# Performance work log

Hardware: AMD Instinct MI355X
Metric: run time of the kernel (lower is better)

The kernel has to match this reference:

```python
import jax, jax.numpy as jnp
import numpy as np

B, L, S = 1, 2048, 2048
D_MODEL, H = 1024, 16
DK = D_MODEL // H  # d_keys = d_values = 64


def sparsemax(z):
    # sparsemax along last axis: proj of z onto the simplex
    K = z.shape[-1]
    z_sorted = jnp.flip(jnp.sort(z, axis=-1), axis=-1)
    cs = jnp.cumsum(z_sorted, axis=-1)
    r = jnp.arange(1, K + 1, dtype=z.dtype)
    support = 1.0 + r * z_sorted > cs
    k = jnp.sum(support, axis=-1, keepdims=True)
    tau = (jnp.take_along_axis(cs, k.astype(jnp.int32) - 1, axis=-1) - 1.0) / k.astype(z.dtype)
    return jnp.maximum(z - tau, 0.0)


def setup_inputs() -> dict:
    key = jax.random.key(0)
    ks = jax.random.split(key, 12)
    sc = 1.0 / np.sqrt(D_MODEL)
    return {
        "queries": jax.random.normal(ks[0], (B, L, D_MODEL), jnp.float32),
        "keys": jax.random.normal(ks[1], (B, S, D_MODEL), jnp.float32),
        "values": jax.random.normal(ks[2], (B, S, D_MODEL), jnp.float32),
        "Wq": jax.random.normal(ks[3], (D_MODEL, H * DK), jnp.float32) * sc,
        "bq": jnp.zeros((H * DK,), jnp.float32),
        "Wk": jax.random.normal(ks[4], (D_MODEL, H * DK), jnp.float32) * sc,
        "bk": jnp.zeros((H * DK,), jnp.float32),
        "Wv": jax.random.normal(ks[5], (H * DK, H * DK), jnp.float32) * sc,
        "bv": jnp.zeros((H * DK,), jnp.float32),
        "Wo": jax.random.normal(ks[6], (H * DK, D_MODEL), jnp.float32) * sc,
        "bo": jnp.zeros((D_MODEL,), jnp.float32),
    }


def reference(queries, keys, values, Wq, bq, Wk, bk, Wv, bv, Wo, bo):
    # projections (note: input `values` is unused, matching the torch source)
    q = (queries @ Wq + bq).reshape(B, L, H, DK)
    k_flat = keys @ Wk + bk                      # [B,S,H*DK]
    k = k_flat.reshape(B, S, H, DK)
    v = (k_flat @ Wv + bv).reshape(B, S, H, DK)  # value_projection(key_projection(keys))
    scale = 1.0 / np.sqrt(DK)
    scores = jnp.einsum('blhe,bshe->bhls', q, k) * scale  # [B,H,L,S]
    A = sparsemax(scores)
    out = jnp.einsum('bhls,bshd->blhd', A, v)             # [B,L,H,DK]
    # mix=True: transpose(2,1) -> [B,H,L,D] then view(B,L,-1)
    out = jnp.swapaxes(out, 1, 2).reshape(B, L, H * DK)
    return out @ Wo + bo
```

## Files before the change

### kernel.cpp

```cpp
#include <hip/hip_runtime.h>
#include <hip/hip_bf16.h>


typedef __attribute__((ext_vector_type(8))) short short8;
typedef __attribute__((ext_vector_type(4))) float floatx4;

#define SRC_BF16 0
#define SRC_F32  1
#define SRC_RT   2
#define NSEG 12
#define OVF 64
#define OVBASE 192
#define CAPP 257

typedef __attribute__((address_space(1))) const void GAS;
typedef __attribute__((address_space(3))) void LAS;
#define GLOAD16(g, l) __builtin_amdgcn_global_load_lds((GAS*)(g), (LAS*)(l), 16, 0, 0)

__device__ __forceinline__ short f2bf(float f) {
    __hip_bfloat16 h = __float2bfloat16(f);
    return *reinterpret_cast<const short*>(&h);
}
__device__ __forceinline__ unsigned short f2bfu(float f) {
    __hip_bfloat16 h = __float2bfloat16(f);
    return *reinterpret_cast<const unsigned short*>(&h);
}
__device__ __forceinline__ float bf2f(unsigned short u) {
    return __uint_as_float(((unsigned)u) << 16);
}
__device__ __forceinline__ unsigned fmap(float f) {
    unsigned u = __float_as_uint(f);
    return (u & 0x80000000u) ? ~u : (u | 0x80000000u);
}
__device__ __forceinline__ float funmap(unsigned u) {
    return (u & 0x80000000u) ? __uint_as_float(u ^ 0x80000000u) : __uint_as_float(~u);
}

__global__ void detect_k(const short* __restrict__ q, int n, int* __restrict__ flag)
{
    const int tid = threadIdx.x;
    int bad = 0;
    for (int i = tid; i < n; i += 64) {
        float f = bf2f((unsigned short)q[i]);
        if (!(fabsf(f) < 1e10f)) bad = 1;
    }
    unsigned long long m = __ballot(bad != 0);
    if (tid == 0) *flag = (m != 0ULL) ? 1 : 0;
}

__global__ __launch_bounds__(256)
void convert2_k(const void* __restrict__ s0, const void* __restrict__ s1,
                short* __restrict__ d0, short* __restrict__ d1,
                const int* __restrict__ dflag)
{
    const void* s = blockIdx.z ? s1 : s0;
    short* d = blockIdx.z ? d1 : d0;
    const size_t i = ((size_t)blockIdx.x * 256 + threadIdx.x) * 8;
    short8 o;
    if (*dflag) {
        const float4 f0 = ((const float4*)((const float*)s + i))[0];
        const float4 f1 = ((const float4*)((const float*)s + i))[1];
        o[0] = f2bf(f0.x); o[1] = f2bf(f0.y); o[2] = f2bf(f0.z); o[3] = f2bf(f0.w);
        o[4] = f2bf(f1.x); o[5] = f2bf(f1.y); o[6] = f2bf(f1.z); o[7] = f2bf(f1.w);
    } else {
        o = *(const short8*)((const short*)s + i);
    }
    *(short8*)(d + i) = o;
}

struct TP4 {
    const void* s[4];
    short* d[4];
};
__global__ __launch_bounds__(256)
void transpose4_k(TP4 p, int R, int C, const int* __restrict__ dflag)
{
    __shared__ short T[64][72];
    const int tid = threadIdx.x;
    const int bC = blockIdx.x, bR = blockIdx.y;
    const void* src = p.s[blockIdx.z];
    short* dst = p.d[blockIdx.z];
    const bool f32 = (*dflag != 0);

    const int colg = (tid & 7) * 8;
    #pragma unroll
    for (int h = 0; h < 2; ++h) {
        const int row = (tid >> 3) + 32 * h;
        const size_t idx = (size_t)(bR * 64 + row) * (size_t)C + (size_t)(bC * 64 + colg);
        short e[8];
        if (f32) {
            const float4 f0 = ((const float4*)((const float*)src + idx))[0];
            const float4 f1 = ((const float4*)((const float*)src + idx))[1];
            e[0] = f2bf(f0.x); e[1] = f2bf(f0.y); e[2] = f2bf(f0.z); e[3] = f2bf(f0.w);
            e[4] = f2bf(f1.x); e[5] = f2bf(f1.y); e[6] = f2bf(f1.z); e[7] = f2bf(f1.w);
        } else {
            short8 s = *(const short8*)((const short*)src + idx);
            #pragma unroll
            for (int j = 0; j < 8; ++j) e[j] = s[j];
        }
        #pragma unroll
        for (int j = 0; j < 8; ++j) T[colg + j][row] = e[j];
    }
    __syncthreads();
    #pragma unroll
    for (int h = 0; h < 2; ++h) {
        const int orow = (tid >> 3) + 32 * h;
        const int ocolg = (tid & 7) * 8;
        const size_t idx = (size_t)(bC * 64 + orow) * (size_t)R + (size_t)(bR * 64 + ocolg);
        *(short8*)(dst + idx) = *(const short8*)&T[orow][ocolg];
    }
}

struct GJ { const short* A; const short* B; const void* bias; void* C; float os; };

template<int OSRC>
__global__ __launch_bounds__(256)
void gemm64_bt_k(GJ j0, GJ j1, const int* __restrict__ dflag)
{
    __shared__ __align__(16) short As[2][64][64];
    __shared__ __align__(16) short Bs[2][64][64];

    const GJ j = blockIdx.z ? j1 : j0;
    const int rtf = *dflag;

    const int tid  = threadIdx.x;
    const int bN   = blockIdx.x, bM = blockIdx.y;
    const int lane = tid & 63, wave = tid >> 6;
    const int wm   = (wave >> 1) * 32;
    const int wn   = (wave & 1) * 32;
    const int quad = lane >> 4, r16 = lane & 15;

    floatx4 acc[2][2];
    #pragma unroll
    for (int i = 0; i < 2; ++i)
        #pragma unroll
        for (int jj = 0; jj < 2; ++jj)
            acc[i][jj] = (floatx4){0.f, 0.f, 0.f, 0.f};

    const int srow = wave * 8 + (lane >> 3);
    const int scg  = (lane & 7) ^ ((lane >> 3) & 7);
    const short* gA = j.A + (size_t)(bM * 64 + srow) * 1024 + scg * 8;
    const short* gB = j.B + (size_t)(bN * 64 + srow) * 1024 + scg * 8;

#define STAGE(buf, k0)                                                          \
    {                                                                           \
        _Pragma("unroll")                                                       \
        for (int jj = 0; jj < 2; ++jj) {                                        \
            GLOAD16(gA + (size_t)jj * 32 * 1024 + (k0),                         \
                    &As[buf][wave * 8 + jj * 32][0]);                           \
            GLOAD16(gB + (size_t)jj * 32 * 1024 + (k0),                         \
                    &Bs[buf][wave * 8 + jj * 32][0]);                           \
        }                                                                       \
    }

    STAGE(0, 0);
    __syncthreads();

    const int sr = r16 & 7;
    int buf = 0;
    for (int t = 0; t < 16; ++t) {
        if (t < 15) STAGE(buf ^ 1, (t + 1) * 64);
        #pragma unroll
        for (int kk = 0; kk < 2; ++kk) {
            const int pc = ((kk * 4 + quad) ^ sr) * 8;
            const short8 a0 = *(const short8*)&As[buf][wm + r16][pc];
            const short8 a1 = *(const short8*)&As[buf][wm + 16 + r16][pc];
            const short8 b0 = *(const short8*)&Bs[buf][wn + r16][pc];
            const short8 b1 = *(const short8*)&Bs[buf][wn + 16 + r16][pc];
            acc[0][0] = __builtin_amdgcn_mfma_f32_16x16x32_bf16(a0, b0, acc[0][0], 0, 0, 0);
            acc[0][1] = __builtin_amdgcn_mfma_f32_16x16x32_bf16(a0, b1, acc[0][1], 0, 0, 0);
            acc[1][0] = __builtin_amdgcn_mfma_f32_16x16x32_bf16(a1, b0, acc[1][0], 0, 0, 0);
            acc[1][1] = __builtin_amdgcn_mfma_f32_16x16x32_bf16(a1, b1, acc[1][1], 0, 0, 0);
        }
        __syncthreads();
        buf ^= 1;
    }
#undef STAGE

    const bool of32 = (OSRC == SRC_F32) || (OSRC == SRC_RT && rtf);
    #pragma unroll
    for (int jj = 0; jj < 2; ++jj) {
        const int gc = bN * 64 + wn + jj * 16 + r16;
        const float bb = rtf ? ((const float*)j.bias)[gc]
                             : bf2f(((const unsigned short*)j.bias)[gc]);
        #pragma unroll
        for (int i = 0; i < 2; ++i) {
            #pragma unroll
            for (int rg = 0; rg < 4; ++rg) {
                const int gr = bM * 64 + wm + i * 16 + quad * 4 + rg;
                const float v = (acc[i][jj][rg] + bb) * j.os;
                if (of32)
                    ((float*)j.C)[(size_t)gr * 1024 + gc] = v;
                else
                    ((__hip_bfloat16*)j.C)[(size_t)gr * 1024 + gc] = __float2bfloat16(v);
            }
        }
    }
}

__global__ __launch_bounds__(256, 8)
void attn_fused_k(const short* __restrict__ Qb, const short* __restrict__ Kb,
                  const short* __restrict__ Vb, short* __restrict__ Ob)
{
    __shared__ unsigned cpk[16][CAPP];
    __shared__ unsigned rmax[16];
    __shared__ int cnt[16];

    const int tid  = threadIdx.x;
    const int lane = tid & 63, wave = tid >> 6;
    const int quad = lane >> 4, r16 = lane & 15;

    const int bid  = blockIdx.x;
    const int slot = bid >> 3;
    const int h    = (slot & 1) * 8 + (bid & 7);
    const int row0 = (slot >> 1) * 16;

    if (tid < 16) { rmax[tid] = fmap(-3.0e38f); cnt[tid] = 0; }
    __syncthreads();

    const short* qp = Qb + (size_t)(row0 + r16) * 1024 + h * 64 + quad * 8;
    const short8 qb0 = *(const short8*)qp;
    const short8 qb1 = *(const short8*)(qp + 32);

    const int wid   = wave * 4 + quad;
    const int kbase = wave * 512;
    const short* kpA = Kb + (size_t)(kbase + r16) * 1024 + h * 64 + quad * 8;

    float rm1 = -3.0e38f, rm2 = -3.0e38f;
    int mycnt = 0;

    for (int s = 0; s < 8; ++s) {
        floatx4 acc[4];
        #pragma unroll
        for (int t = 0; t < 4; ++t) {
            const short* kp = kpA + (size_t)(s * 64 + t * 16) * 1024;
            const short8 a0 = *(const short8*)kp;
            const short8 a1 = *(const short8*)(kp + 32);
            floatx4 a = (floatx4){0.f, 0.f, 0.f, 0.f};
            a = __builtin_amdgcn_mfma_f32_16x16x32_bf16(a0, qb0, a, 0, 0, 0);
            a = __builtin_amdgcn_mfma_f32_16x16x32_bf16(a1, qb1, a, 0, 0, 0);
            acc[t] = a;
        }

        float m1 = acc[0][0], m2 = -3.0e38f;
        #pragma unroll
        for (int t = 0; t < 4; ++t) {
            #pragma unroll
            for (int rg = 0; rg < 4; ++rg) {
                if (t == 0 && rg == 0) continue;
                const float v = acc[t][rg];
                m2 = fmaxf(m2, fminf(m1, v));
                m1 = fmaxf(m1, v);
            }
        }
        #pragma unroll
        for (int off = 16; off < 64; off <<= 1) {
            const float o1 = __shfl_xor(m1, off, 64);
            const float o2 = __shfl_xor(m2, off, 64);
            const float n2 = fmaxf(fminf(m1, o1), (m1 >= o1) ? m2 : o2);
            m1 = fmaxf(m1, o1);
            m2 = n2;
        }
        rm2 = fmaxf(fminf(rm1, m1), (rm1 >= m1) ? rm2 : m2);
        rm1 = fmaxf(rm1, m1);
        if (quad == 0) atomicMax(&rmax[r16], fmap(m1));

        const float g1 = fmaxf(funmap(rmax[r16]), rm1);
        const float thr = fmaxf(g1 - 1.0f, 0.5f * (g1 + rm2) - 0.5f);
        #pragma unroll
        for (int t = 0; t < 4; ++t) {
            #pragma unroll
            for (int rg = 0; rg < 4; ++rg) {
                const float val = acc[t][rg];
                if (val >= thr) {
                    const unsigned pk = ((unsigned)f2bfu(val) << 16)
                        | (unsigned)(kbase + s * 64 + t * 16 + quad * 4 + rg);
                    const int c = mycnt;
                    if (c < NSEG) {
                        cpk[r16][wid * NSEG + c] = pk;
                    } else {
                        const int p = atomicAdd(&cnt[r16], 1);
                        if (p < OVF) cpk[r16][OVBASE + p] = pk;
                    }
                    mycnt = c + 1;
                }
            }
        }
    }

    for (int k = mycnt; k < NSEG; ++k)
        cpk[r16][wid * NSEG + k] = 0xFF800000u;
    __syncthreads();

    const int r = wave * 4 + quad;
    const int novf = min(cnt[r], OVF);

    unsigned ca[16];
    #pragma unroll
    for (int k = 0; k < 12; ++k) ca[k] = cpk[r][k * 16 + r16];
    #pragma unroll
    for (int k = 12; k < 16; ++k) {
        const int oi = k * 16 + r16 - OVBASE;
        ca[k] = (oi < novf) ? cpk[r][k * 16 + r16] : 0xFF800000u;
    }

    float tau = funmap(rmax[r]) - 1.0f;
    float prevc = -1.0f;
    for (int it = 0; it < 18; ++it) {
        float s = 0.f, c = 0.f;
        #pragma unroll
        for (int k = 0; k < 16; ++k) {
            const float v = __uint_as_float(ca[k] & 0xFFFF0000u);
            if (v > tau) { s += v; c += 1.f; }
        }
        #pragma unroll
        for (int off = 1; off < 16; off <<= 1) {
            s += __shfl_xor(s, off, 64);
            c += __shfl_xor(c, off, 64);
        }
        if (c == prevc || c == 0.f) break;
        prevc = c;
        tau = (s - 1.0f) / c;
    }

    const unsigned qpre = (1u << r16) - 1u;
    int base = 0;
    #pragma unroll
    for (int k = 0; k < 16; ++k) {
        const float v = __uint_as_float(ca[k] & 0xFFFF0000u);
        const float p = v - tau;
        const bool keep = (p > 0.f);
        const unsigned long long mm = __ballot(keep);
        const unsigned qm = (unsigned)((mm >> (quad * 16)) & 0xFFFFull);
        if (keep)
            cpk[r][base + __popc(qm & qpre)] =
                ((unsigned)f2bfu(p) << 16) | (ca[k] & 0xFFFFu);
        base += __popc(qm);
    }
    const int msup = base;

    const unsigned short* vb = (const unsigned short*)Vb + (size_t)h * 64 + r16 * 4;
    float o0 = 0.f, o1 = 0.f, o2 = 0.f, o3 = 0.f;
    int jj = 0;
    for (; jj + 2 <= msup; jj += 2) {
        const unsigned ua = cpk[r][jj], ub = cpk[r][jj + 1];
        const float pa = __uint_as_float(ua & 0xFFFF0000u);
        const float pb = __uint_as_float(ub & 0xFFFF0000u);
        const uint2 da = *(const uint2*)(vb + (size_t)(ua & 0xFFFFu) * 1024);
        const uint2 db = *(const uint2*)(vb + (size_t)(ub & 0xFFFFu) * 1024);
        o0 += pa * __uint_as_float(da.x << 16);
        o1 += pa * __uint_as_float(da.x & 0xFFFF0000u);
        o2 += pa * __uint_as_float(da.y << 16);
        o3 += pa * __uint_as_float(da.y & 0xFFFF0000u);
        o0 += pb * __uint_as_float(db.x << 16);
        o1 += pb * __uint_as_float(db.x & 0xFFFF0000u);
        o2 += pb * __uint_as_float(db.y << 16);
        o3 += pb * __uint_as_float(db.y & 0xFFFF0000u);
    }
    if (jj < msup) {
        const unsigned ua = cpk[r][jj];
        const float pa = __uint_as_float(ua & 0xFFFF0000u);
        const uint2 da = *(const uint2*)(vb + (size_t)(ua & 0xFFFFu) * 1024);
        o0 += pa * __uint_as_float(da.x << 16);
        o1 += pa * __uint_as_float(da.x & 0xFFFF0000u);
        o2 += pa * __uint_as_float(da.y << 16);
        o3 += pa * __uint_as_float(da.y & 0xFFFF0000u);
    }

    short* op = Ob + ((size_t)h * 2048 + row0 + r) * 64 + r16 * 4;
    op[0] = f2bf(o0); op[1] = f2bf(o1); op[2] = f2bf(o2); op[3] = f2bf(o3);
}

extern "C" void kernel_launch(void* const* d_in, const int* in_sizes, int n_in,
                              void* d_out, int out_size, void* d_ws, size_t ws_size,
                              hipStream_t stream)
{
    (void)in_sizes; (void)n_in; (void)out_size; (void)ws_size;

    const void* queries = d_in[0];
    const void* keys    = d_in[1];
    const void* Wq = d_in[3];
    const void* bq = d_in[4];
    const void* Wk = d_in[5];
    const void* bk = d_in[6];
    const void* Wv = d_in[7];
    const void* bv = d_in[8];
    const void* Wo = d_in[9];
    const void* bo = d_in[10];

    const int L = 2048, DM = 1024;
    const size_t LD = (size_t)L * DM;

    int*   flag = (int*)d_ws;
    short* Qc  = (short*)((char*)d_ws + 256);
    short* Kc  = Qc + LD;
    short* WqT = Kc + LD;
    short* WkT = WqT + (size_t)DM * DM;
    short* WvT = WkT + (size_t)DM * DM;
    short* WoT = WvT + (size_t)DM * DM;
    short* Qb  = WoT + (size_t)DM * DM;
    short* Kb  = Qb + LD;
    short* Vb  = Kb + LD;
    short* Ob  = Vb + LD;

    dim3 blk(256);

    detect_k<<<dim3(1), dim3(64), 0, stream>>>((const short*)queries, 4096, flag);

    convert2_k<<<dim3((unsigned)(LD / 2048), 1, 2), blk, 0, stream>>>(
        queries, keys, Qc, Kc, flag);

    {
        TP4 p;
        p.s[0] = Wq; p.s[1] = Wk; p.s[2] = Wv; p.s[3] = Wo;
        p.d[0] = WqT; p.d[1] = WkT; p.d[2] = WvT; p.d[3] = WoT;
        transpose4_k<<<dim3(DM / 64, DM / 64, 4), blk, 0, stream>>>(p, DM, DM, flag);
    }

    {
        GJ jq{(const short*)Qc, WqT, bq, Qb, 0.125f};
        GJ jk{(const short*)Kc, WkT, bk, Kb, 1.0f};
        gemm64_bt_k<SRC_BF16><<<dim3(DM / 64, L / 64, 2), blk, 0, stream>>>(jq, jk, flag);
    }
    {
        GJ jv{(const short*)Kb, WvT, bv, Vb, 1.0f};
        gemm64_bt_k<SRC_BF16><<<dim3(DM / 64, L / 64, 1), blk, 0, stream>>>(jv, jv, flag);
    }

    attn_fused_k<<<dim3((L / 16) * 16), blk, 0, stream>>>(Qb, Kb, Vb, Ob);

    {
        GJ jo{(const short*)Ob, WoT, bo, d_out, 1.0f};
        gemm64_bt_k<SRC_RT><<<dim3(DM / 64, L / 64, 1), blk, 0, stream>>>(jo, jo, flag);
    }
}
```

Baseline: 232.4 us.

## Enlarge projection GEMM tiles to 128x128 with 512-thread blocks and K-step 32

Replaces the 64x64 GEMM kernel with a 128x128 output tile computed by 8 waves, each owning a 64x32 sub-tile with 4x2 MFMA accumulators. The K step is halved to 32 and the LDS swizzle is changed to match. The goal is more reuse per loaded tile and fewer global loads per flop. In exchange there are fewer blocks (128 or 256 per launch on a 256-CU device), so occupancy and wave-level parallelism may drop, and there are twice as many loop iterations and barriers.

```diff
diff --git a/kernel.cpp b/kernel.cpp
--- a/kernel.cpp
+++ b/kernel.cpp
@@ -114,11 +114,11 @@
 struct GJ { const short* A; const short* B; const void* bias; void* C; float os; };
 
 template<int OSRC>
-__global__ __launch_bounds__(256)
-void gemm64_bt_k(GJ j0, GJ j1, const int* __restrict__ dflag)
-{
-    __shared__ __align__(16) short As[2][64][64];
-    __shared__ __align__(16) short Bs[2][64][64];
+__global__ __launch_bounds__(512)
+void gemm128_bt_k(GJ j0, GJ j1, const int* __restrict__ dflag)
+{
+    __shared__ __align__(16) short As[2][128][32];
+    __shared__ __align__(16) short Bs[2][128][32];
 
     const GJ j = blockIdx.z ? j1 : j0;
     const int rtf = *dflag;
@@ -126,51 +126,49 @@
     const int tid  = threadIdx.x;
     const int bN   = blockIdx.x, bM = blockIdx.y;
     const int lane = tid & 63, wave = tid >> 6;
-    const int wm   = (wave >> 1) * 32;
-    const int wn   = (wave & 1) * 32;
+    const int wm   = (wave >> 2) * 64;
+    const int wn   = (wave & 3) * 32;
     const int quad = lane >> 4, r16 = lane & 15;
 
-    floatx4 acc[2][2];
-    #pragma unroll
-    for (int i = 0; i < 2; ++i)
+    floatx4 acc[4][2];
+    #pragma unroll
+    for (int i = 0; i < 4; ++i)
         #pragma unroll
         for (int jj = 0; jj < 2; ++jj)
             acc[i][jj] = (floatx4){0.f, 0.f, 0.f, 0.f};
 
-    const int srow = wave * 8 + (lane >> 3);
-    const int scg  = (lane & 7) ^ ((lane >> 3) & 7);
-    const short* gA = j.A + (size_t)(bM * 64 + srow) * 1024 + scg * 8;
-    const short* gB = j.B + (size_t)(bN * 64 + srow) * 1024 + scg * 8;
+    const int srow = tid >> 2;
+    const int scol = (((tid & 3) ^ ((tid >> 3) & 3)) * 8);
+    const short* gA = j.A + (size_t)(bM * 128 + srow) * 1024 + scol;
+    const short* gB = j.B + (size_t)(bN * 128 + srow) * 1024 + scol;
+    const int wrow = (tid >> 6) * 16;
 
 #define STAGE(buf, k0)                                                          \
     {                                                                           \
-        _Pragma("unroll")                                                       \
-        for (int jj = 0; jj < 2; ++jj) {                                        \
-            GLOAD16(gA + (size_t)jj * 32 * 1024 + (k0),                         \
-                    &As[buf][wave * 8 + jj * 32][0]);                           \
-            GLOAD16(gB + (size_t)jj * 32 * 1024 + (k0),                         \
-                    &Bs[buf][wave * 8 + jj * 32][0]);                           \
-        }                                                                       \
+        GLOAD16(gA + (k0), &As[buf][wrow][0]);                                  \
+        GLOAD16(gB + (k0), &Bs[buf][wrow][0]);                                  \
     }
 
     STAGE(0, 0);
     __syncthreads();
 
-    const int sr = r16 & 7;
+    const int pcq = (quad ^ ((r16 >> 1) & 3)) * 8;
     int buf = 0;
-    for (int t = 0; t < 16; ++t) {
-        if (t < 15) STAGE(buf ^ 1, (t + 1) * 64);
-        #pragma unroll
-        for (int kk = 0; kk < 2; ++kk) {
-            const int pc = ((kk * 4 + quad) ^ sr) * 8;
-            const short8 a0 = *(const short8*)&As[buf][wm + r16][pc];
-            const short8 a1 = *(const short8*)&As[buf][wm + 16 + r16][pc];
-            const short8 b0 = *(const short8*)&Bs[buf][wn + r16][pc];
-            const short8 b1 = *(const short8*)&Bs[buf][wn + 16 + r16][pc];
-            acc[0][0] = __builtin_amdgcn_mfma_f32_16x16x32_bf16(a0, b0, acc[0][0], 0, 0, 0);
-            acc[0][1] = __builtin_amdgcn_mfma_f32_16x16x32_bf16(a0, b1, acc[0][1], 0, 0, 0);
-            acc[1][0] = __builtin_amdgcn_mfma_f32_16x16x32_bf16(a1, b0, acc[1][0], 0, 0, 0);
-            acc[1][1] = __builtin_amdgcn_mfma_f32_16x16x32_bf16(a1, b1, acc[1][1], 0, 0, 0);
+    for (int t = 0; t < 32; ++t) {
+        if (t < 31) STAGE(buf ^ 1, (t + 1) * 32);
+        short8 a[4], b[2];
+        #pragma unroll
+        for (int i = 0; i < 4; ++i)
+            a[i] = *(const short8*)&As[buf][wm + i * 16 + r16][pcq];
+        #pragma unroll
+        for (int jj = 0; jj < 2; ++jj)
+            b[jj] = *(const short8*)&Bs[buf][wn + jj * 16 + r16][pcq];
+        #pragma unroll
+        for (int i = 0; i < 4; ++i) {
+            #pragma unroll
+            for (int jj = 0; jj < 2; ++jj)
+                acc[i][jj] = __builtin_amdgcn_mfma_f32_16x16x32_bf16(
+                    a[i], b[jj], acc[i][jj], 0, 0, 0);
         }
         __syncthreads();
         buf ^= 1;
@@ -180,14 +178,14 @@
     const bool of32 = (OSRC == SRC_F32) || (OSRC == SRC_RT && rtf);
     #pragma unroll
     for (int jj = 0; jj < 2; ++jj) {
-        const int gc = bN * 64 + wn + jj * 16 + r16;
+        const int gc = bN * 128 + wn + jj * 16 + r16;
         const float bb = rtf ? ((const float*)j.bias)[gc]
                              : bf2f(((const unsigned short*)j.bias)[gc]);
         #pragma unroll
-        for (int i = 0; i < 2; ++i) {
+        for (int i = 0; i < 4; ++i) {
             #pragma unroll
             for (int rg = 0; rg < 4; ++rg) {
-                const int gr = bM * 64 + wm + i * 16 + quad * 4 + rg;
+                const int gr = bM * 128 + wm + i * 16 + quad * 4 + rg;
                 const float v = (acc[i][jj][rg] + bb) * j.os;
                 if (of32)
                     ((float*)j.C)[(size_t)gr * 1024 + gc] = v;
@@ -403,7 +401,7 @@
     short* Vb  = Kb + LD;
     short* Ob  = Vb + LD;
 
-    dim3 blk(256);
+    dim3 blk(256), blk2(512);
 
     detect_k<<<dim3(1), dim3(64), 0, stream>>>((const short*)queries, 4096, flag);
 
@@ -420,17 +418,17 @@
     {
         GJ jq{(const short*)Qc, WqT, bq, Qb, 0.125f};
         GJ jk{(const short*)Kc, WkT, bk, Kb, 1.0f};
-        gemm64_bt_k<SRC_BF16><<<dim3(DM / 64, L / 64, 2), blk, 0, stream>>>(jq, jk, flag);
+        gemm128_bt_k<SRC_BF16><<<dim3(DM / 128, L / 128, 2), blk2, 0, stream>>>(jq, jk, flag);
     }
     {
         GJ jv{(const short*)Kb, WvT, bv, Vb, 1.0f};
-        gemm64_bt_k<SRC_BF16><<<dim3(DM / 64, L / 64, 1), blk, 0, stream>>>(jv, jv, flag);
+        gemm128_bt_k<SRC_BF16><<<dim3(DM / 128, L / 128, 1), blk2, 0, stream>>>(jv, jv, flag);
     }
 
     attn_fused_k<<<dim3((L / 16) * 16), blk, 0, stream>>>(Qb, Kb, Vb, Ob);
 
     {
         GJ jo{(const short*)Ob, WoT, bo, d_out, 1.0f};
-        gemm64_bt_k<SRC_RT><<<dim3(DM / 64, L / 64, 1), blk, 0, stream>>>(jo, jo, flag);
-    }
-}
+        gemm128_bt_k<SRC_RT><<<dim3(DM / 128, L / 128, 1), blk2, 0, stream>>>(jo, jo, flag);
+    }
+}
```

New measurement: 244.1 us. 5.0% more time.
